# Kernel optimization log

Hardware: AMD Instinct MI355X
Metric: run time of the kernel (lower is better)

The kernel has to match this reference:

```python
import jax, jax.numpy as jnp
import numpy as np

B, S, D, H, L = 4, 2048, 256, 4, 2
DK = D // H
V, T = 32000, 1000


def setup_inputs() -> dict:
    key = jax.random.key(0)
    ks = jax.random.split(key, 20)
    sc = 0.02
    event_emb = jax.random.normal(ks[0], (V, D), jnp.float32) * sc
    event_emb = event_emb.at[0].set(0.0)  # padding_idx=0
    time_emb = jax.random.normal(ks[1], (T, D), jnp.float32) * sc
    inp = {
        "x": jax.random.randint(ks[2], (B, S), 0, V, jnp.int32),
        "time_deltas": jax.random.randint(ks[3], (B, S), 0, T, jnp.int32),
        "mask": jax.random.randint(ks[4], (B, S), 0, 2, jnp.int32),
        "event_emb": event_emb,
        "time_emb": time_emb,
        "Wq": jax.random.normal(ks[5], (L, D, D), jnp.float32) * sc,
        "bq": jnp.zeros((L, D), jnp.float32),
        "Wk": jax.random.normal(ks[6], (L, D, D), jnp.float32) * sc,
        "bk": jnp.zeros((L, D), jnp.float32),
        "Wv": jax.random.normal(ks[7], (L, D, D), jnp.float32) * sc,
        "bv": jnp.zeros((L, D), jnp.float32),
        "time_proj": jax.random.normal(ks[8], (L, T, H), jnp.float32) * sc,
        "Wo": jax.random.normal(ks[9], (L, D, D), jnp.float32) * sc,
        "bo": jnp.zeros((L, D), jnp.float32),
        "ln_g": jnp.ones((L, D), jnp.float32),
        "ln_b": jnp.zeros((L, D), jnp.float32),
        "Wc1": jax.random.normal(ks[10], (D, D // 2), jnp.float32) * sc,
        "bc1": jnp.zeros((D // 2,), jnp.float32),
        "Wc2": jax.random.normal(ks[11], (D // 2, 1), jnp.float32) * sc,
        "bc2": jnp.zeros((1,), jnp.float32),
    }
    return inp


def _layernorm(h, g, b, eps=1e-5):
    mu = jnp.mean(h, -1, keepdims=True)
    var = jnp.mean(jnp.square(h - mu), -1, keepdims=True)
    return (h - mu) * jax.lax.rsqrt(var + eps) * g + b


def _attn(h, t_bins, mask, Wq, bq, Wk, bk, Wv, bv, tp, Wo, bo):
    b, s, d = h.shape
    q = (h @ Wq + bq).reshape(b, s, H, DK)
    k = (h @ Wk + bk).reshape(b, s, H, DK)
    v = (h @ Wv + bv).reshape(b, s, H, DK)
    scores = jnp.einsum("bqhd,bkhd->bhqk", q, k) / np.sqrt(DK).astype(np.float32)
    time_bias = tp[t_bins]  # [b,s,H] -> bias per key position
    scores = scores + jnp.transpose(time_bias, (0, 2, 1))[:, :, None, :]
    scores = jnp.where(mask[:, None, None, :] == 0, -1e9, scores)
    attn = jax.nn.softmax(scores, axis=-1)
    ctx = jnp.einsum("bhqk,bkhd->bqhd", attn, v).reshape(b, s, d)
    return ctx @ Wo + bo


def reference(x, time_deltas, mask, event_emb, time_emb, Wq, bq, Wk, bk, Wv, bv,
              time_proj, Wo, bo, ln_g, ln_b, Wc1, bc1, Wc2, bc2):
    t_bins = jnp.clip(time_deltas, 0, T - 1)
    h = event_emb[x] + time_emb[t_bins]
    for l in range(L):
        h = _attn(h, t_bins, mask, Wq[l], bq[l], Wk[l], bk[l], Wv[l], bv[l],
                  time_proj[l], Wo[l], bo[l])
        h = _layernorm(h, ln_g[l], ln_b[l])
    last = h[:, -1, :]
    hid = jax.nn.relu(last @ Wc1 + bc1)
    return jax.nn.sigmoid(hid @ Wc2 + bc2)
```

## Files before the change

kernel.cpp:

```cpp
#include <hip/hip_runtime.h>
#include <math.h>

namespace {

constexpr int NB = 4, NS = 2048, ND = 256, NH = 4, NDK = 64, NL = 2, NT = 1000;
constexpr float L2E = 1.44269504089f;
constexpr float QSCALE = 0.125f * L2E;

typedef short bfx8 __attribute__((ext_vector_type(8)));
typedef float f32x4 __attribute__((ext_vector_type(4)));
typedef float f32x16 __attribute__((ext_vector_type(16)));

static __device__ __forceinline__ short f2bf(float f) {
  union { float f; unsigned u; } v; v.f = f;
  unsigned u = v.u;
  unsigned r = (u + 0x7fffu + ((u >> 16) & 1u)) >> 16;
  return (short)r;
}
static __device__ __forceinline__ float bf2f(short s) {
  union { float f; unsigned u; } v; v.u = ((unsigned)(unsigned short)s) << 16;
  return v.f;
}
static __device__ __forceinline__ float exp2_hw(float x) {
  float r;
  asm("v_exp_f32 %0, %1" : "=v"(r) : "v"(x));
  return r;
}
static __device__ __forceinline__ unsigned cvt_pk_bf16(float lo, float hi) {
  unsigned d;
  asm("v_cvt_pk_bf16_f32 %0, %1, %2" : "=v"(d) : "v"(lo), "v"(hi));
  return d;
}

__global__ __launch_bounds__(256) void k_packw(const float* __restrict__ Wq,
                                               const float* __restrict__ Wk,
                                               const float* __restrict__ Wv,
                                               const float* __restrict__ Wo,
                                               const float* __restrict__ bq,
                                               const float* __restrict__ bk,
                                               const float* __restrict__ bv,
                                               short* __restrict__ wqkvT,
                                               short* __restrict__ woT,
                                               float* __restrict__ bqkv) {
  __shared__ float t[64][65];
  int z = blockIdx.z, l = z >> 2, mat = z & 3;
  const float* src;
  short* dst;
  float scale = 1.f;
  if (mat == 0)      { src = Wq + (size_t)l * 65536; dst = wqkvT + (size_t)l * 768 * 256; scale = QSCALE; }
  else if (mat == 1) { src = Wk + (size_t)l * 65536; dst = wqkvT + (size_t)l * 768 * 256 + 256 * 256; }
  else if (mat == 2) { src = Wv + (size_t)l * 65536; dst = wqkvT + (size_t)l * 768 * 256 + 512 * 256; }
  else               { src = Wo + (size_t)l * 65536; dst = woT + (size_t)l * 65536; }
  int k0 = blockIdx.x * 64, n0 = blockIdx.y * 64;
  int c = threadIdx.x & 63, r4 = threadIdx.x >> 6;
  #pragma unroll
  for (int rr = 0; rr < 64; rr += 4) t[rr + r4][c] = src[(size_t)(k0 + rr + r4) * 256 + n0 + c];
  __syncthreads();
  #pragma unroll
  for (int rr = 0; rr < 64; rr += 4) {
    int n = rr + r4;
    dst[(size_t)(n0 + n) * 256 + k0 + c] = f2bf(t[c][n] * scale);
  }
  if (mat == 0 && blockIdx.x == 0 && blockIdx.y == 0) {
    for (int cc = threadIdx.x; cc < 768; cc += 256) {
      float v = cc < 256 ? bq[l * 256 + cc] * QSCALE
                         : (cc < 512 ? bk[l * 256 + cc - 256] : bv[l * 256 + cc - 512]);
      bqkv[l * 768 + cc] = v;
    }
  }
}

__global__ __launch_bounds__(256) void k_embed(const int* __restrict__ x,
                                               const int* __restrict__ td,
                                               const float* __restrict__ ee,
                                               const float* __restrict__ te,
                                               short* __restrict__ hb) {
  int lane = threadIdx.x & 63, r4 = threadIdx.x >> 6;
  int row = blockIdx.x * 4 + r4;
  int xi = x[row];
  int tb = td[row];
  tb = tb < 0 ? 0 : (tb >= NT ? NT - 1 : tb);
  float4 e = ((const float4*)&ee[(size_t)xi * ND])[lane];
  float4 tv = ((const float4*)&te[(size_t)tb * ND])[lane];
  short4 ob;
  ob.x = f2bf(e.x + tv.x); ob.y = f2bf(e.y + tv.y);
  ob.z = f2bf(e.z + tv.z); ob.w = f2bf(e.w + tv.w);
  ((short4*)&hb[(size_t)row * ND])[lane] = ob;
}

template <int OUT_BF16>
__global__ __launch_bounds__(256) void k_gemm(const short* __restrict__ A,
                                              const short* __restrict__ BT,
                                              const float* __restrict__ bias,
                                              void* __restrict__ C, int ldc,
                                              int mb_mul, int mb_add, int n_base) {
  constexpr int LP = 76;
  __shared__ short at[64][LP];
  __shared__ short bt[128][LP];
  int tid = threadIdx.x;
  int w = tid >> 6, lane = tid & 63, ln15 = lane & 15, g = lane >> 4;
  int m0 = (blockIdx.x * mb_mul + mb_add) * 64;
  int n0 = n_base + blockIdx.y * 128;
  int srow = tid >> 2, scol = (tid & 3) * 16;
  int brow = tid >> 1, bcol = (tid & 1) * 32;

  f32x4 acc[8];
  #pragma unroll
  for (int nt = 0; nt < 8; ++nt) acc[nt] = (f32x4){0.f, 0.f, 0.f, 0.f};

  bfx8 a0, a1, b0, b1, b2, b3;
  auto LOAD = [&](int kk0) {
    const short* as = &A[(size_t)(m0 + srow) * 256 + kk0 + scol];
    a0 = *(const bfx8*)as; a1 = *(const bfx8*)(as + 8);
    const short* bs = &BT[(size_t)(n0 + brow) * 256 + kk0 + bcol];
    b0 = *(const bfx8*)bs; b1 = *(const bfx8*)(bs + 8);
    b2 = *(const bfx8*)(bs + 16); b3 = *(const bfx8*)(bs + 24);
  };
  LOAD(0);
  for (int kk0 = 0; kk0 < 256; kk0 += 64) {
    __syncthreads();
    *(bfx8*)&at[srow][scol] = a0; *(bfx8*)&at[srow][scol + 8] = a1;
    *(bfx8*)&bt[brow][bcol] = b0; *(bfx8*)&bt[brow][bcol + 8] = b1;
    *(bfx8*)&bt[brow][bcol + 16] = b2; *(bfx8*)&bt[brow][bcol + 24] = b3;
    __syncthreads();
    if (kk0 + 64 < 256) LOAD(kk0 + 64);
    #pragma unroll
    for (int ks = 0; ks < 2; ++ks) {
      bfx8 af = *(const bfx8*)&at[w * 16 + ln15][ks * 32 + g * 8];
      #pragma unroll
      for (int nt = 0; nt < 8; ++nt) {
        bfx8 bf = *(const bfx8*)&bt[nt * 16 + ln15][ks * 32 + g * 8];
        acc[nt] = __builtin_amdgcn_mfma_f32_16x16x32_bf16(af, bf, acc[nt], 0, 0, 0);
      }
    }
  }

  #pragma unroll
  for (int nt = 0; nt < 8; ++nt) {
    int col = n0 + nt * 16 + ln15;
    float bb = bias[col];
    #pragma unroll
    for (int r = 0; r < 4; ++r) {
      int row = m0 + w * 16 + g * 4 + r;
      float val = acc[nt][r] + bb;
      if (OUT_BF16) ((short*)C)[(size_t)row * ldc + col] = f2bf(val);
      else          ((float*)C)[(size_t)row * ldc + col] = val;
    }
  }
}

__global__ __launch_bounds__(256) void k_pmerge(const short* __restrict__ partO,
                                                const float* __restrict__ partML,
                                                const short* __restrict__ BT,
                                                const float* __restrict__ bias,
                                                short* __restrict__ C) {
  constexpr int LP = 76;
  constexpr int NC = 2;
  __shared__ short at[64][LP];
  __shared__ short bt[128][LP];
  int tid = threadIdx.x;
  int w = tid >> 6, lane = tid & 63, ln15 = lane & 15, g = lane >> 4;
  int m0 = blockIdx.x * 64;
  int n0 = blockIdx.y * 128;
  int srow = tid >> 2, scol = (tid & 3) * 16;
  int brow = tid >> 1, bcol = (tid & 1) * 32;

  int grow = m0 + srow;
  int b = grow >> 11, s = grow & 2047;

  f32x4 acc[8];
  #pragma unroll
  for (int nt = 0; nt < 8; ++nt) acc[nt] = (f32x4){0.f, 0.f, 0.f, 0.f};

  bfx8 a0, a1, b0_, b1_, b2_, b3_;
  auto LOAD = [&](int kk0) {
    int hh2 = kk0 >> 6;
    size_t rbase = (size_t)(b * NH + hh2) * NS + s;
    float2 ml[NC];
    float M = -1e30f;
    #pragma unroll
    for (int c = 0; c < NC; ++c) {
      ml[c] = *(const float2*)&partML[(rbase + (size_t)c * 16 * NS) * 2];
      M = fmaxf(M, ml[c].x);
    }
    float wgt[NC], L = 0.f;
    #pragma unroll
    for (int c = 0; c < NC; ++c) { wgt[c] = exp2_hw(ml[c].x - M); L += ml[c].y * wgt[c]; }
    float inv = 1.f / L;
    float av[16];
    #pragma unroll
    for (int i = 0; i < 16; ++i) av[i] = 0.f;
    #pragma unroll
    for (int c = 0; c < NC; ++c) {
      float wc = wgt[c] * inv;
      size_t row = rbase + (size_t)c * 16 * NS;
      union { int4 v; short sh[8]; } ua, ub;
      ua.v = *(const int4*)&partO[row * 64 + scol];
      ub.v = *(const int4*)&partO[row * 64 + scol + 8];
      #pragma unroll
      for (int i = 0; i < 8; ++i) {
        av[i]     = fmaf(bf2f(ua.sh[i]), wc, av[i]);
        av[8 + i] = fmaf(bf2f(ub.sh[i]), wc, av[8 + i]);
      }
    }
    union { bfx8 v; short sh[8]; } pa, pb;
    #pragma unroll
    for (int i = 0; i < 8; ++i) { pa.sh[i] = f2bf(av[i]); pb.sh[i] = f2bf(av[8 + i]); }
    a0 = pa.v; a1 = pb.v;
    const short* bs = &BT[(size_t)(n0 + brow) * 256 + kk0 + bcol];
    b0_ = *(const bfx8*)bs; b1_ = *(const bfx8*)(bs + 8);
    b2_ = *(const bfx8*)(bs + 16); b3_ = *(const bfx8*)(bs + 24);
  };
  LOAD(0);
  for (int kk0 = 0; kk0 < 256; kk0 += 64) {
    __syncthreads();
    *(bfx8*)&at[srow][scol] = a0; *(bfx8*)&at[srow][scol + 8] = a1;
    *(bfx8*)&bt[brow][bcol] = b0_; *(bfx8*)&bt[brow][bcol + 8] = b1_;
    *(bfx8*)&bt[brow][bcol + 16] = b2_; *(bfx8*)&bt[brow][bcol + 24] = b3_;
    __syncthreads();
    if (kk0 + 64 < 256) LOAD(kk0 + 64);
    #pragma unroll
    for (int ks = 0; ks < 2; ++ks) {
      bfx8 af = *(const bfx8*)&at[w * 16 + ln15][ks * 32 + g * 8];
      #pragma unroll
      for (int nt = 0; nt < 8; ++nt) {
        bfx8 bf = *(const bfx8*)&bt[nt * 16 + ln15][ks * 32 + g * 8];
        acc[nt] = __builtin_amdgcn_mfma_f32_16x16x32_bf16(af, bf, acc[nt], 0, 0, 0);
      }
    }
  }

  #pragma unroll
  for (int nt = 0; nt < 8; ++nt) {
    int col = n0 + nt * 16 + ln15;
    float bb = bias[col];
    #pragma unroll
    for (int r = 0; r < 4; ++r) {
      int row = m0 + w * 16 + g * 4 + r;
      C[(size_t)row * 256 + col] = f2bf(acc[nt][r] + bb);
    }
  }
}

__global__ __launch_bounds__(256) void k_frag(const short* __restrict__ qkv,
                                              const int* __restrict__ td,
                                              const int* __restrict__ mask,
                                              const float* __restrict__ tp,
                                              short* __restrict__ vT,
                                              float* __restrict__ sbias_g) {
  __shared__ short vl[64][72];
  int tile = blockIdx.x, hh = blockIdx.y, b = blockIdx.z;
  int t = threadIdx.x;
  int k0 = tile * 64;
  {
    int key = t >> 2, dg = (t & 3) * 16;
    const short* vsrc = &qkv[(size_t)(b * NS + k0 + key) * 768 + 512 + hh * NDK + dg];
    bfx8 v0 = *(const bfx8*)vsrc, v1 = *(const bfx8*)(vsrc + 8);
    *(bfx8*)&vl[key][dg] = v0;
    *(bfx8*)&vl[key][dg + 8] = v1;
  }
  if (t < 64) {
    int kk = k0 + t;
    int tb = td[b * NS + kk];
    tb = tb < 0 ? 0 : (tb >= NT ? NT - 1 : tb);
    sbias_g[(size_t)(b * NH + hh) * NS + kk] = mask[b * NS + kk] ? tp[tb * NH + hh] * L2E : -1e9f;
  }
  __syncthreads();
  int dim = t >> 2, c0 = (t & 3) * 16;
  short outv[16];
  #pragma unroll
  for (int j = 0; j < 16; ++j) outv[j] = vl[c0 + j][dim];
  short* dst = &vT[(((size_t)(b * NH + hh) * 32 + tile) * 64 + dim) * 64 + c0];
  *(int4*)dst = *(const int4*)outv;
  *(int4*)(dst + 8) = *(const int4*)(outv + 8);
}

__global__ __launch_bounds__(256) void k_attn(const short* __restrict__ qkv,
                                              const short* __restrict__ vT,
                                              const float* __restrict__ sbias_g,
                                              short* __restrict__ partO,
                                              float* __restrict__ partML,
                                              int q_base, int qcount, int nchunk) {
  constexpr int LP = 76;
  __shared__ short kt[64][LP];
  __shared__ short vt[64][LP];
  __shared__ float sbias[64];

  int tid = threadIdx.x;
  int w = tid >> 6, lane = tid & 63, q31 = lane & 31, hl = lane >> 5;
  int b = blockIdx.z, hh = blockIdx.y;
  int bh = b * NH + hh;
  int qtile = blockIdx.x / nchunk;
  int chunk = blockIdx.x - qtile * nchunk;
  int niter = NS / (64 * nchunk);
  int tbase = chunk * niter;
  int q0 = q_base + qtile * 128;
  int qq = q0 + w * 32 + q31;

  bfx8 aq[4];
  #pragma unroll
  for (int ki = 0; ki < 4; ++ki)
    aq[ki] = *(const bfx8*)&qkv[(size_t)(b * NS + qq) * 768 + hh * NDK + ki * 16 + hl * 8];

  f32x16 o[2];
  #pragma unroll
  for (int dt = 0; dt < 2; ++dt)
    #pragma unroll
    for (int i = 0; i < 16; ++i) o[dt][i] = 0.f;
  float m = -1e30f, lsum = 0.f;

  int srow = tid >> 2, scg = (tid & 3) * 16;

  bfx8 kr0, kr1, vr0, vr1;
  float br = 0.f;
  auto loadset = [&](int it) {
    int tt = tbase + it;
    int k0 = tt * 64;
    const short* ksrc = &qkv[(size_t)(b * NS + k0 + srow) * 768 + 256 + hh * NDK + scg];
    kr0 = *(const bfx8*)ksrc; kr1 = *(const bfx8*)(ksrc + 8);
    const short* vsrc = &vT[(((size_t)bh * 32 + tt) * 64 + srow) * 64 + scg];
    vr0 = *(const bfx8*)vsrc; vr1 = *(const bfx8*)(vsrc + 8);
    if (tid < 64) br = sbias_g[(size_t)bh * NS + k0 + tid];
  };

  loadset(0);
  for (int it = 0; it < niter; ++it) {
    __syncthreads();
    *(bfx8*)&kt[srow][scg] = kr0;
    *(bfx8*)&kt[srow][scg + 8] = kr1;
    *(bfx8*)&vt[srow][scg] = vr0;
    *(bfx8*)&vt[srow][scg + 8] = vr1;
    if (tid < 64) sbias[tid] = br;
    __syncthreads();
    if (it + 1 < niter) loadset(it + 1);

    f32x16 c[2];
    #pragma unroll
    for (int kt2 = 0; kt2 < 2; ++kt2)
      #pragma unroll
      for (int i = 0; i < 16; ++i) c[kt2][i] = 0.f;
    __builtin_amdgcn_s_setprio(1);
    #pragma unroll
    for (int kt2 = 0; kt2 < 2; ++kt2) {
      #pragma unroll
      for (int ki = 0; ki < 4; ++ki) {
        bfx8 kf = *(const bfx8*)&kt[kt2 * 32 + q31][ki * 16 + hl * 8];
        c[kt2] = __builtin_amdgcn_mfma_f32_32x32x16_bf16(kf, aq[ki], c[kt2], 0, 0, 0);
      }
    }
    __builtin_amdgcn_s_setprio(0);

    #pragma unroll
    for (int kt2 = 0; kt2 < 2; ++kt2) {
      #pragma unroll
      for (int rg = 0; rg < 4; ++rg) {
        float4 bb = *(const float4*)&sbias[kt2 * 32 + rg * 8 + hl * 4];
        c[kt2][rg * 4 + 0] += bb.x; c[kt2][rg * 4 + 1] += bb.y;
        c[kt2][rg * 4 + 2] += bb.z; c[kt2][rg * 4 + 3] += bb.w;
      }
    }
    float rm = c[0][0];
    #pragma unroll
    for (int kt2 = 0; kt2 < 2; ++kt2)
      #pragma unroll
      for (int i = 0; i < 16; ++i) rm = fmaxf(rm, c[kt2][i]);
    rm = fmaxf(rm, __shfl_xor(rm, 32, 64));
    if (__any(rm > m + 10.f)) {
      float nm = fmaxf(m, rm);
      float scl = exp2_hw(m - nm);
      m = nm;
      lsum *= scl;
      #pragma unroll
      for (int dt = 0; dt < 2; ++dt)
        #pragma unroll
        for (int i = 0; i < 16; ++i) o[dt][i] *= scl;
    }
    float ts = 0.f;
    #pragma unroll
    for (int kt2 = 0; kt2 < 2; ++kt2)
      #pragma unroll
      for (int i = 0; i < 16; ++i) { c[kt2][i] = exp2_hw(c[kt2][i] - m); ts += c[kt2][i]; }
    lsum += ts;

    __builtin_amdgcn_s_setprio(1);
    #pragma unroll
    for (int kt2 = 0; kt2 < 2; ++kt2) {
      #pragma unroll
      for (int ks = 0; ks < 2; ++ks) {
        unsigned pa0 = cvt_pk_bf16(c[kt2][8 * ks + 0], c[kt2][8 * ks + 1]);
        unsigned pa1 = cvt_pk_bf16(c[kt2][8 * ks + 2], c[kt2][8 * ks + 3]);
        unsigned pb0 = cvt_pk_bf16(c[kt2][8 * ks + 4], c[kt2][8 * ks + 5]);
        unsigned pb1 = cvt_pk_bf16(c[kt2][8 * ks + 6], c[kt2][8 * ks + 7]);
        asm volatile("v_permlane32_swap_b32 %0, %1" : "+v"(pa0), "+v"(pb0));
        asm volatile("v_permlane32_swap_b32 %0, %1" : "+v"(pa1), "+v"(pb1));
        union { unsigned u[4]; bfx8 v; } pf;
        pf.u[0] = pa0; pf.u[1] = pa1; pf.u[2] = pb0; pf.u[3] = pb1;
        #pragma unroll
        for (int dt = 0; dt < 2; ++dt) {
          bfx8 vf = *(const bfx8*)&vt[dt * 32 + q31][kt2 * 32 + ks * 16 + hl * 8];
          o[dt] = __builtin_amdgcn_mfma_f32_32x32x16_bf16(vf, pf.v, o[dt], 0, 0, 0);
        }
      }
    }
    __builtin_amdgcn_s_setprio(0);
  }

  lsum += __shfl_xor(lsum, 32, 64);

  size_t rowi = (size_t)(chunk * 16 + bh) * qcount + qtile * 128 + w * 32 + q31;
  #pragma unroll
  for (int dt = 0; dt < 2; ++dt) {
    #pragma unroll
    for (int rg = 0; rg < 4; ++rg) {
      int2 pk;
      pk.x = (int)cvt_pk_bf16(o[dt][rg * 4 + 0], o[dt][rg * 4 + 1]);
      pk.y = (int)cvt_pk_bf16(o[dt][rg * 4 + 2], o[dt][rg * 4 + 3]);
      *(int2*)&partO[rowi * 64 + dt * 32 + rg * 8 + hl * 4] = pk;
    }
  }
  if (hl == 0) { partML[rowi * 2] = m; partML[rowi * 2 + 1] = lsum; }
}

__global__ __launch_bounds__(256) void k_amerge(const short* __restrict__ partO,
                                                const float* __restrict__ partML,
                                                short* __restrict__ ctx,
                                                int q_base, int qcount, int nchunk) {
  int b = blockIdx.z, hh = blockIdx.y;
  int qi = blockIdx.x * 64 + (threadIdx.x >> 2);
  int d0 = (threadIdx.x & 3) * 16;
  int bh = b * NH + hh;
  float M = -1e30f;
  for (int c = 0; c < nchunk; ++c)
    M = fmaxf(M, partML[((size_t)(c * 16 + bh) * qcount + qi) * 2]);
  float L = 0.f;
  float acc[16];
  #pragma unroll
  for (int i = 0; i < 16; ++i) acc[i] = 0.f;
  for (int c = 0; c < nchunk; ++c) {
    size_t row = (size_t)(c * 16 + bh) * qcount + qi;
    float mc = partML[row * 2];
    float lc = partML[row * 2 + 1];
    float s = exp2_hw(mc - M);
    L += lc * s;
    union { int4 v; short sh[8]; } u0, u1;
    u0.v = *(const int4*)&partO[row * 64 + d0];
    u1.v = *(const int4*)&partO[row * 64 + d0 + 8];
    #pragma unroll
    for (int i = 0; i < 8; ++i) {
      acc[i]     += bf2f(u0.sh[i]) * s;
      acc[8 + i] += bf2f(u1.sh[i]) * s;
    }
  }
  float inv = 1.f / L;
  short res[16];
  #pragma unroll
  for (int i = 0; i < 16; ++i) res[i] = f2bf(acc[i] * inv);
  short* dst = &ctx[(size_t)(b * NS + q_base + qi) * ND + hh * NDK + d0];
  *(int4*)dst = *(const int4*)res;
  *(int4*)(dst + 8) = *(const int4*)(res + 8);
}

__global__ __launch_bounds__(256) void k_ln(float* __restrict__ h,
                                            short* __restrict__ hb,
                                            const float* __restrict__ g_,
                                            const float* __restrict__ b_, int q_base) {
  int lane = threadIdx.x & 63, r4 = threadIdx.x >> 6;
  size_t row = (size_t)blockIdx.y * NS + q_base + blockIdx.x * 4 + r4;
  float4 v = ((const float4*)&h[row * ND])[lane];
  float s = v.x + v.y + v.z + v.w;
  #pragma unroll
  for (int off = 1; off < 64; off <<= 1) s += __shfl_xor(s, off, 64);
  float mu = s * (1.f / ND);
  float dx = v.x - mu, dy = v.y - mu, dz = v.z - mu, dw = v.w - mu;
  float q = dx * dx + dy * dy + dz * dz + dw * dw;
  #pragma unroll
  for (int off = 1; off < 64; off <<= 1) q += __shfl_xor(q, off, 64);
  float rr = rsqrtf(q * (1.f / ND) + 1e-5f);
  float4 gg = ((const float4*)g_)[lane];
  float4 bb = ((const float4*)b_)[lane];
  float4 o;
  o.x = dx * rr * gg.x + bb.x;
  o.y = dy * rr * gg.y + bb.y;
  o.z = dz * rr * gg.z + bb.z;
  o.w = dw * rr * gg.w + bb.w;
  ((float4*)&h[row * ND])[lane] = o;
  short4 ob; ob.x = f2bf(o.x); ob.y = f2bf(o.y); ob.z = f2bf(o.z); ob.w = f2bf(o.w);
  ((short4*)&hb[row * ND])[lane] = ob;
}

__global__ __launch_bounds__(256) void k_lnb(const short* __restrict__ in,
                                             short* __restrict__ hb,
                                             const float* __restrict__ g_,
                                             const float* __restrict__ b_) {
  int lane = threadIdx.x & 63, r4 = threadIdx.x >> 6;
  size_t row = (size_t)blockIdx.y * NS + blockIdx.x * 4 + r4;
  short4 sv = ((const short4*)&in[row * ND])[lane];
  float vx = bf2f(sv.x), vy = bf2f(sv.y), vz = bf2f(sv.z), vw = bf2f(sv.w);
  float s = vx + vy + vz + vw;
  #pragma unroll
  for (int off = 1; off < 64; off <<= 1) s += __shfl_xor(s, off, 64);
  float mu = s * (1.f / ND);
  float dx = vx - mu, dy = vy - mu, dz = vz - mu, dw = vw - mu;
  float q = dx * dx + dy * dy + dz * dz + dw * dw;
  #pragma unroll
  for (int off = 1; off < 64; off <<= 1) q += __shfl_xor(q, off, 64);
  float rr = rsqrtf(q * (1.f / ND) + 1e-5f);
  float4 gg = ((const float4*)g_)[lane];
  float4 bb = ((const float4*)b_)[lane];
  short4 ob;
  ob.x = f2bf(dx * rr * gg.x + bb.x);
  ob.y = f2bf(dy * rr * gg.y + bb.y);
  ob.z = f2bf(dz * rr * gg.z + bb.z);
  ob.w = f2bf(dw * rr * gg.w + bb.w);
  ((short4*)&hb[row * ND])[lane] = ob;
}

__global__ __launch_bounds__(128) void k_head(const float* __restrict__ h,
                                              const float* __restrict__ Wc1,
                                              const float* __restrict__ bc1,
                                              const float* __restrict__ Wc2,
                                              const float* __restrict__ bc2,
                                              float* __restrict__ out) {
  __shared__ float red[128];
  int j = threadIdx.x;
  int b = blockIdx.x;
  const float* last = &h[(size_t)(b * NS + NS - 1) * ND];
  float acc = bc1[j];
  for (int d = 0; d < ND; ++d) acc = fmaf(last[d], Wc1[d * 128 + j], acc);
  acc = fmaxf(acc, 0.f);
  red[j] = acc * Wc2[j];
  __syncthreads();
  for (int off = 64; off > 0; off >>= 1) {
    if (j < off) red[j] += red[j + off];
    __syncthreads();
  }
  if (j == 0) out[b] = 1.f / (1.f + __expf(-(red[0] + bc2[0])));
}

}

extern "C" void kernel_launch(void* const* d_in, const int* in_sizes, int n_in,
                              void* d_out, int out_size, void* d_ws, size_t ws_size,
                              hipStream_t stream) {
  const int* x = (const int*)d_in[0];
  const int* td = (const int*)d_in[1];
  const int* mask = (const int*)d_in[2];
  const float* ee = (const float*)d_in[3];
  const float* te = (const float*)d_in[4];
  const float* Wq = (const float*)d_in[5];
  const float* bq = (const float*)d_in[6];
  const float* Wk = (const float*)d_in[7];
  const float* bk = (const float*)d_in[8];
  const float* Wv = (const float*)d_in[9];
  const float* bv = (const float*)d_in[10];
  const float* tp = (const float*)d_in[11];
  const float* Wo = (const float*)d_in[12];
  const float* bo = (const float*)d_in[13];
  const float* lng = (const float*)d_in[14];
  const float* lnb = (const float*)d_in[15];
  const float* Wc1 = (const float*)d_in[16];
  const float* bc1 = (const float*)d_in[17];
  const float* Wc2 = (const float*)d_in[18];
  const float* bc2 = (const float*)d_in[19];
  float* out = (float*)d_out;

  char* ws = (char*)d_ws;
  const size_t M = (size_t)NB * NS;
  short* qkv     = (short*)(ws);
  float* h       = (float*)(ws + (12 << 20));
  short* hb      = (short*)(ws + (20 << 20));
  short* vT      = (short*)(ws + (24 << 20));
  float* sbias_g = (float*)(ws + (28 << 20));
  short* wqkvT   = (short*)(ws + (28 << 20) + (128 << 10));
  short* woT     = (short*)(ws + (28 << 20) + (896 << 10));
  float* bqkv    = (float*)(ws + (28 << 20) + (1152 << 10));
  short* partO   = (short*)(ws + (30 << 20));
  float* partML  = (float*)(ws + (47 << 20));
  short* hraw    = (short*)(ws + (48 << 20));
  short* ctx1    = vT;

  k_packw<<<dim3(4, 4, 8), 256, 0, stream>>>(Wq, Wk, Wv, Wo, bq, bk, bv, wqkvT, woT, bqkv);
  k_embed<<<NB * NS / 4, 256, 0, stream>>>(x, td, ee, te, hb);

  for (int l = 0; l < NL; ++l) {
    const short* wqkvTl = wqkvT + (size_t)l * 768 * 256;
    const short* woTl = woT + (size_t)l * 65536;
    const float* bqkvl = bqkv + (size_t)l * 768;
    const float* bol = bo + (size_t)l * ND;
    const float* tpl = tp + (size_t)l * NT * NH;
    const float* lngl = lng + (size_t)l * ND;
    const float* lnbl = lnb + (size_t)l * ND;
    const bool last = (l == NL - 1);

    if (!last) {
      k_gemm<1><<<dim3(M / 64, 6), 256, 0, stream>>>(hb, wqkvTl, bqkvl, qkv, 768, 1, 0, 0);
    } else {
      k_gemm<1><<<dim3(M / 64, 4), 256, 0, stream>>>(hb, wqkvTl, bqkvl, qkv, 768, 1, 0, 256);
      k_gemm<1><<<dim3(NB, 2), 256, 0, stream>>>(hb, wqkvTl, bqkvl, qkv, 768, 32, 31, 0);
    }

    k_frag<<<dim3(32, NH, NB), 256, 0, stream>>>(qkv, td, mask, tpl, vT, sbias_g);

    if (!last) {
      k_attn<<<dim3(16 * 2, NH, NB), 256, 0, stream>>>(qkv, vT, sbias_g,
                                                       partO, partML, 0, NS, 2);
      k_pmerge<<<dim3(M / 64, 2), 256, 0, stream>>>(partO, partML, woTl, bol, hraw);
      k_lnb<<<dim3(NS / 4, NB), 256, 0, stream>>>(hraw, hb, lngl, lnbl);
    } else {
      k_attn<<<dim3(16, NH, NB), 256, 0, stream>>>(qkv, vT, sbias_g,
                                                   partO, partML, NS - 128, 128, 16);
      k_amerge<<<dim3(2, NH, NB), 256, 0, stream>>>(partO, partML, ctx1, NS - 128, 128, 16);
      k_gemm<0><<<dim3(NB, 2), 256, 0, stream>>>(ctx1, woTl, bol, h, 256, 32, 31, 0);
      k_ln<<<dim3(1, NB), 256, 0, stream>>>(h, hb, lngl, lnbl, NS - 4);
    }
  }

  k_head<<<NB, 128, 0, stream>>>(h, Wc1, bc1, Wc2, bc2, out);
}
```

Measured before the change: 120.5 us.

## Fuse weight packing with embedding, merge+Wo GEMM, and LN with head

Merges weight packing and embedding gather into one launch, folds the last-layer split-KV merge into the Wo projection GEMM's A-operand load, and combines the final layernorm with the classifier head. Launch count drops from several small kernels to fewer. The aim is to remove launch overhead and intermediate ctx/h round trips on the tail, which is dominated by tiny grids. In exchange the merge work is recomputed per N-block in the GEMM, and the head now does LN with shared-memory reductions.

```diff
diff --git a/kernel.cpp b/kernel.cpp
--- a/kernel.cpp
+++ b/kernel.cpp
@@ -32,60 +32,62 @@
   return d;
 }
 
-__global__ __launch_bounds__(256) void k_packw(const float* __restrict__ Wq,
-                                               const float* __restrict__ Wk,
-                                               const float* __restrict__ Wv,
-                                               const float* __restrict__ Wo,
-                                               const float* __restrict__ bq,
-                                               const float* __restrict__ bk,
-                                               const float* __restrict__ bv,
-                                               short* __restrict__ wqkvT,
-                                               short* __restrict__ woT,
-                                               float* __restrict__ bqkv) {
-  __shared__ float t[64][65];
-  int z = blockIdx.z, l = z >> 2, mat = z & 3;
-  const float* src;
-  short* dst;
-  float scale = 1.f;
-  if (mat == 0)      { src = Wq + (size_t)l * 65536; dst = wqkvT + (size_t)l * 768 * 256; scale = QSCALE; }
-  else if (mat == 1) { src = Wk + (size_t)l * 65536; dst = wqkvT + (size_t)l * 768 * 256 + 256 * 256; }
-  else if (mat == 2) { src = Wv + (size_t)l * 65536; dst = wqkvT + (size_t)l * 768 * 256 + 512 * 256; }
-  else               { src = Wo + (size_t)l * 65536; dst = woT + (size_t)l * 65536; }
-  int k0 = blockIdx.x * 64, n0 = blockIdx.y * 64;
-  int c = threadIdx.x & 63, r4 = threadIdx.x >> 6;
-  #pragma unroll
-  for (int rr = 0; rr < 64; rr += 4) t[rr + r4][c] = src[(size_t)(k0 + rr + r4) * 256 + n0 + c];
-  __syncthreads();
-  #pragma unroll
-  for (int rr = 0; rr < 64; rr += 4) {
-    int n = rr + r4;
-    dst[(size_t)(n0 + n) * 256 + k0 + c] = f2bf(t[c][n] * scale);
-  }
-  if (mat == 0 && blockIdx.x == 0 && blockIdx.y == 0) {
-    for (int cc = threadIdx.x; cc < 768; cc += 256) {
-      float v = cc < 256 ? bq[l * 256 + cc] * QSCALE
-                         : (cc < 512 ? bk[l * 256 + cc - 256] : bv[l * 256 + cc - 512]);
-      bqkv[l * 768 + cc] = v;
-    }
-  }
-}
-
-__global__ __launch_bounds__(256) void k_embed(const int* __restrict__ x,
-                                               const int* __restrict__ td,
-                                               const float* __restrict__ ee,
-                                               const float* __restrict__ te,
-                                               short* __restrict__ hb) {
-  int lane = threadIdx.x & 63, r4 = threadIdx.x >> 6;
-  int row = blockIdx.x * 4 + r4;
-  int xi = x[row];
-  int tb = td[row];
-  tb = tb < 0 ? 0 : (tb >= NT ? NT - 1 : tb);
-  float4 e = ((const float4*)&ee[(size_t)xi * ND])[lane];
-  float4 tv = ((const float4*)&te[(size_t)tb * ND])[lane];
-  short4 ob;
-  ob.x = f2bf(e.x + tv.x); ob.y = f2bf(e.y + tv.y);
-  ob.z = f2bf(e.z + tv.z); ob.w = f2bf(e.w + tv.w);
-  ((short4*)&hb[(size_t)row * ND])[lane] = ob;
+__global__ __launch_bounds__(256) void k_packem(const int* __restrict__ x,
+                                                const int* __restrict__ td,
+                                                const float* __restrict__ ee,
+                                                const float* __restrict__ te,
+                                                short* __restrict__ hb,
+                                                const float* __restrict__ Wq,
+                                                const float* __restrict__ Wk,
+                                                const float* __restrict__ Wv,
+                                                const float* __restrict__ Wo,
+                                                const float* __restrict__ bq,
+                                                const float* __restrict__ bk,
+                                                const float* __restrict__ bv,
+                                                short* __restrict__ wqkvT,
+                                                short* __restrict__ woT,
+                                                float* __restrict__ bqkv) {
+  if (blockIdx.x < 128) {
+    __shared__ float t[64][65];
+    int bi = blockIdx.x;
+    int z = bi >> 4, l = z >> 2, mat = z & 3;
+    const float* src;
+    short* dst;
+    float scale = 1.f;
+    if (mat == 0)      { src = Wq + (size_t)l * 65536; dst = wqkvT + (size_t)l * 768 * 256; scale = QSCALE; }
+    else if (mat == 1) { src = Wk + (size_t)l * 65536; dst = wqkvT + (size_t)l * 768 * 256 + 256 * 256; }
+    else if (mat == 2) { src = Wv + (size_t)l * 65536; dst = wqkvT + (size_t)l * 768 * 256 + 512 * 256; }
+    else               { src = Wo + (size_t)l * 65536; dst = woT + (size_t)l * 65536; }
+    int k0 = (bi & 3) * 64, n0 = ((bi >> 2) & 3) * 64;
+    int c = threadIdx.x & 63, r4 = threadIdx.x >> 6;
+    #pragma unroll
+    for (int rr = 0; rr < 64; rr += 4) t[rr + r4][c] = src[(size_t)(k0 + rr + r4) * 256 + n0 + c];
+    __syncthreads();
+    #pragma unroll
+    for (int rr = 0; rr < 64; rr += 4) {
+      int n = rr + r4;
+      dst[(size_t)(n0 + n) * 256 + k0 + c] = f2bf(t[c][n] * scale);
+    }
+    if (mat == 0 && (bi & 15) == 0) {
+      for (int cc = threadIdx.x; cc < 768; cc += 256) {
+        float v = cc < 256 ? bq[l * 256 + cc] * QSCALE
+                           : (cc < 512 ? bk[l * 256 + cc - 256] : bv[l * 256 + cc - 512]);
+        bqkv[l * 768 + cc] = v;
+      }
+    }
+  } else {
+    int lane = threadIdx.x & 63, r4 = threadIdx.x >> 6;
+    int row = (blockIdx.x - 128) * 4 + r4;
+    int xi = x[row];
+    int tb = td[row];
+    tb = tb < 0 ? 0 : (tb >= NT ? NT - 1 : tb);
+    float4 e = ((const float4*)&ee[(size_t)xi * ND])[lane];
+    float4 tv = ((const float4*)&te[(size_t)tb * ND])[lane];
+    short4 ob;
+    ob.x = f2bf(e.x + tv.x); ob.y = f2bf(e.y + tv.y);
+    ob.z = f2bf(e.z + tv.z); ob.w = f2bf(e.w + tv.w);
+    ((short4*)&hb[(size_t)row * ND])[lane] = ob;
+  }
 }
 
 template <int OUT_BF16>
@@ -238,6 +240,101 @@
     for (int r = 0; r < 4; ++r) {
       int row = m0 + w * 16 + g * 4 + r;
       C[(size_t)row * 256 + col] = f2bf(acc[nt][r] + bb);
+    }
+  }
+}
+
+__global__ __launch_bounds__(256) void k_gmerge(const short* __restrict__ partO,
+                                                const float* __restrict__ partML,
+                                                const short* __restrict__ BT,
+                                                const float* __restrict__ bias,
+                                                float* __restrict__ C) {
+  constexpr int LP = 76;
+  constexpr int NC = 16;
+  __shared__ short at[64][LP];
+  __shared__ short bt[128][LP];
+  int tid = threadIdx.x;
+  int w = tid >> 6, lane = tid & 63, ln15 = lane & 15, g = lane >> 4;
+  int m0 = (blockIdx.x * 32 + 31) * 64;
+  int n0 = blockIdx.y * 128;
+  int srow = tid >> 2, scol = (tid & 3) * 16;
+  int brow = tid >> 1, bcol = (tid & 1) * 32;
+
+  int grow = m0 + srow;
+  int b = grow >> 11, s = grow & 2047;
+  int qloc = s - (NS - 128);
+
+  f32x4 acc[8];
+  #pragma unroll
+  for (int nt = 0; nt < 8; ++nt) acc[nt] = (f32x4){0.f, 0.f, 0.f, 0.f};
+
+  bfx8 a0, a1, b0_, b1_, b2_, b3_;
+  auto LOAD = [&](int kk0) {
+    int hh2 = kk0 >> 6;
+    size_t rbase = (size_t)(b * NH + hh2) * 128 + qloc;
+    float M = -1e30f;
+    float mls[NC], lls[NC];
+    #pragma unroll
+    for (int c = 0; c < NC; ++c) {
+      float2 ml = *(const float2*)&partML[(rbase + (size_t)c * 16 * 128) * 2];
+      mls[c] = ml.x; lls[c] = ml.y;
+      M = fmaxf(M, ml.x);
+    }
+    float L = 0.f, wgt[NC];
+    #pragma unroll
+    for (int c = 0; c < NC; ++c) { wgt[c] = exp2_hw(mls[c] - M); L += lls[c] * wgt[c]; }
+    float inv = 1.f / L;
+    float av[16];
+    #pragma unroll
+    for (int i = 0; i < 16; ++i) av[i] = 0.f;
+    #pragma unroll
+    for (int c = 0; c < NC; ++c) {
+      float wc = wgt[c] * inv;
+      size_t row = rbase + (size_t)c * 16 * 128;
+      union { int4 v; short sh[8]; } ua, ub;
+      ua.v = *(const int4*)&partO[row * 64 + scol];
+      ub.v = *(const int4*)&partO[row * 64 + scol + 8];
+      #pragma unroll
+      for (int i = 0; i < 8; ++i) {
+        av[i]     = fmaf(bf2f(ua.sh[i]), wc, av[i]);
+        av[8 + i] = fmaf(bf2f(ub.sh[i]), wc, av[8 + i]);
+      }
+    }
+    union { bfx8 v; short sh[8]; } pa, pb;
+    #pragma unroll
+    for (int i = 0; i < 8; ++i) { pa.sh[i] = f2bf(av[i]); pb.sh[i] = f2bf(av[8 + i]); }
+    a0 = pa.v; a1 = pb.v;
+    const short* bs = &BT[(size_t)(n0 + brow) * 256 + kk0 + bcol];
+    b0_ = *(const bfx8*)bs; b1_ = *(const bfx8*)(bs + 8);
+    b2_ = *(const bfx8*)(bs + 16); b3_ = *(const bfx8*)(bs + 24);
+  };
+  LOAD(0);
+  for (int kk0 = 0; kk0 < 256; kk0 += 64) {
+    __syncthreads();
+    *(bfx8*)&at[srow][scol] = a0; *(bfx8*)&at[srow][scol + 8] = a1;
+    *(bfx8*)&bt[brow][bcol] = b0_; *(bfx8*)&bt[brow][bcol + 8] = b1_;
+    *(bfx8*)&bt[brow][bcol + 16] = b2_; *(bfx8*)&bt[brow][bcol + 24] = b3_;
+    __syncthreads();
+    if (kk0 + 64 < 256) LOAD(kk0 + 64);
+    #pragma unroll
+    for (int ks = 0; ks < 2; ++ks) {
+      bfx8 af = *(const bfx8*)&at[w * 16 + ln15][ks * 32 + g * 8];
+      #pragma unroll
+      for (int nt = 0; nt < 8; ++nt) {
+        bfx8 bf = *(const bfx8*)&bt[nt * 16 + ln15][ks * 32 + g * 8];
+        acc[nt] = __builtin_amdgcn_mfma_f32_16x16x32_bf16(af, bf, acc[nt], 0, 0, 0);
+      }
+    }
+  }
+
+  #pragma unroll
+  for (int nt = 0; nt < 8; ++nt) {
+    int col = n0 + nt * 16 + ln15;
+    float bb = bias[col];
+    #pragma unroll
+    for (int r = 0; r < 4; ++r) {
+      int row = m0 + w * 16 + g * 4 + r;
+      C[(size_t)row * 256 + col] = acc[nt][r] + bb;
     }
   }
 }
@@ -421,73 +518,6 @@
   if (hl == 0) { partML[rowi * 2] = m; partML[rowi * 2 + 1] = lsum; }
 }
 
-__global__ __launch_bounds__(256) void k_amerge(const short* __restrict__ partO,
-                                                const float* __restrict__ partML,
-                                                short* __restrict__ ctx,
-                                                int q_base, int qcount, int nchunk) {
-  int b = blockIdx.z, hh = blockIdx.y;
-  int qi = blockIdx.x * 64 + (threadIdx.x >> 2);
-  int d0 = (threadIdx.x & 3) * 16;
-  int bh = b * NH + hh;
-  float M = -1e30f;
-  for (int c = 0; c < nchunk; ++c)
-    M = fmaxf(M, partML[((size_t)(c * 16 + bh) * qcount + qi) * 2]);
-  float L = 0.f;
-  float acc[16];
-  #pragma unroll
-  for (int i = 0; i < 16; ++i) acc[i] = 0.f;
-  for (int c = 0; c < nchunk; ++c) {
-    size_t row = (size_t)(c * 16 + bh) * qcount + qi;
-    float mc = partML[row * 2];
-    float lc = partML[row * 2 + 1];
-    float s = exp2_hw(mc - M);
-    L += lc * s;
-    union { int4 v; short sh[8]; } u0, u1;
-    u0.v = *(const int4*)&partO[row * 64 + d0];
-    u1.v = *(const int4*)&partO[row * 64 + d0 + 8];
-    #pragma unroll
-    for (int i = 0; i < 8; ++i) {
-      acc[i]     += bf2f(u0.sh[i]) * s;
-      acc[8 + i] += bf2f(u1.sh[i]) * s;
-    }
-  }
-  float inv = 1.f / L;
-  short res[16];
-  #pragma unroll
-  for (int i = 0; i < 16; ++i) res[i] = f2bf(acc[i] * inv);
-  short* dst = &ctx[(size_t)(b * NS + q_base + qi) * ND + hh * NDK + d0];
-  *(int4*)dst = *(const int4*)res;
-  *(int4*)(dst + 8) = *(const int4*)(res + 8);
-}
-
-__global__ __launch_bounds__(256) void k_ln(float* __restrict__ h,
-                                            short* __restrict__ hb,
-                                            const float* __restrict__ g_,
-                                            const float* __restrict__ b_, int q_base) {
-  int lane = threadIdx.x & 63, r4 = threadIdx.x >> 6;
-  size_t row = (size_t)blockIdx.y * NS + q_base + blockIdx.x * 4 + r4;
-  float4 v = ((const float4*)&h[row * ND])[lane];
-  float s = v.x + v.y + v.z + v.w;
-  #pragma unroll
-  for (int off = 1; off < 64; off <<= 1) s += __shfl_xor(s, off, 64);
-  float mu = s * (1.f / ND);
-  float dx = v.x - mu, dy = v.y - mu, dz = v.z - mu, dw = v.w - mu;
-  float q = dx * dx + dy * dy + dz * dz + dw * dw;
-  #pragma unroll
-  for (int off = 1; off < 64; off <<= 1) q += __shfl_xor(q, off, 64);
-  float rr = rsqrtf(q * (1.f / ND) + 1e-5f);
-  float4 gg = ((const float4*)g_)[lane];
-  float4 bb = ((const float4*)b_)[lane];
-  float4 o;
-  o.x = dx * rr * gg.x + bb.x;
-  o.y = dy * rr * gg.y + bb.y;
-  o.z = dz * rr * gg.z + bb.z;
-  o.w = dw * rr * gg.w + bb.w;
-  ((float4*)&h[row * ND])[lane] = o;
-  short4 ob; ob.x = f2bf(o.x); ob.y = f2bf(o.y); ob.z = f2bf(o.z); ob.w = f2bf(o.w);
-  ((short4*)&hb[row * ND])[lane] = ob;
-}
-
 __global__ __launch_bounds__(256) void k_lnb(const short* __restrict__ in,
                                              short* __restrict__ hb,
                                              const float* __restrict__ g_,
@@ -515,20 +545,44 @@
   ((short4*)&hb[row * ND])[lane] = ob;
 }
 
-__global__ __launch_bounds__(128) void k_head(const float* __restrict__ h,
-                                              const float* __restrict__ Wc1,
-                                              const float* __restrict__ bc1,
-                                              const float* __restrict__ Wc2,
-                                              const float* __restrict__ bc2,
-                                              float* __restrict__ out) {
-  __shared__ float red[128];
-  int j = threadIdx.x;
-  int b = blockIdx.x;
-  const float* last = &h[(size_t)(b * NS + NS - 1) * ND];
-  float acc = bc1[j];
-  for (int d = 0; d < ND; ++d) acc = fmaf(last[d], Wc1[d * 128 + j], acc);
-  acc = fmaxf(acc, 0.f);
-  red[j] = acc * Wc2[j];
+__global__ __launch_bounds__(256) void k_lnhead(const float* __restrict__ h,
+                                                const float* __restrict__ g_,
+                                                const float* __restrict__ b_,
+                                                const float* __restrict__ Wc1,
+                                                const float* __restrict__ bc1,
+                                                const float* __restrict__ Wc2,
+                                                const float* __restrict__ bc2,
+                                                float* __restrict__ out) {
+  __shared__ float rowv[256];
+  __shared__ float red[256];
+  int b = blockIdx.x, j = threadIdx.x;
+  float v = h[(size_t)(b * NS + NS - 1) * ND + j];
+  red[j] = v;
+  __syncthreads();
+  for (int off = 128; off > 0; off >>= 1) {
+    if (j < off) red[j] += red[j + off];
+    __syncthreads();
+  }
+  float mu = red[0] * (1.f / ND);
+  __syncthreads();
+  float d = v - mu;
+  red[j] = d * d;
+  __syncthreads();
+  for (int off = 128; off > 0; off >>= 1) {
+    if (j < off) red[j] += red[j + off];
+    __syncthreads();
+  }
+  float rr = rsqrtf(red[0] * (1.f / ND) + 1e-5f);
+  rowv[j] = d * rr * g_[j] + b_[j];
+  __syncthreads();
+  float hid = 0.f;
+  if (j < 128) {
+    hid = bc1[j];
+    for (int dd = 0; dd < ND; ++dd) hid = fmaf(rowv[dd], Wc1[dd * 128 + j], hid);
+    hid = fmaxf(hid, 0.f) * Wc2[j];
+  }
+  __syncthreads();
+  red[j] = j < 128 ? hid : 0.f;
   __syncthreads();
   for (int off = 64; off > 0; off >>= 1) {
     if (j < off) red[j] += red[j + off];
@@ -577,10 +631,10 @@
   short* partO   = (short*)(ws + (30 << 20));
   float* partML  = (float*)(ws + (47 << 20));
   short* hraw    = (short*)(ws + (48 << 20));
-  short* ctx1    = vT;
-
-  k_packw<<<dim3(4, 4, 8), 256, 0, stream>>>(Wq, Wk, Wv, Wo, bq, bk, bv, wqkvT, woT, bqkv);
-  k_embed<<<NB * NS / 4, 256, 0, stream>>>(x, td, ee, te, hb);
+
+  k_packem<<<128 + NB * NS / 4, 256, 0, stream>>>(x, td, ee, te, hb,
+                                                  Wq, Wk, Wv, Wo, bq, bk, bv,
+                                                  wqkvT, woT, bqkv);
 
   for (int l = 0; l < NL; ++l) {
     const short* wqkvTl = wqkvT + (size_t)l * 768 * 256;
@@ -609,11 +663,8 @@
     } else {
       k_attn<<<dim3(16, NH, NB), 256, 0, stream>>>(qkv, vT, sbias_g,
                                                    partO, partML, NS - 128, 128, 16);
-      k_amerge<<<dim3(2, NH, NB), 256, 0, stream>>>(partO, partML, ctx1, NS - 128, 128, 16);
-      k_gemm<0><<<dim3(NB, 2), 256, 0, stream>>>(ctx1, woTl, bol, h, 256, 32, 31, 0);
-      k_ln<<<dim3(1, NB), 256, 0, stream>>>(h, hb, lngl, lnbl, NS - 4);
-    }
-  }
-
-  k_head<<<NB, 128, 0, stream>>>(h, Wc1, bc1, Wc2, bc2, out);
-}
+      k_gmerge<<<dim3(NB, 2), 256, 0, stream>>>(partO, partML, woTl, bol, h);
+      k_lnhead<<<NB, 256, 0, stream>>>(h, lngl, lnbl, Wc1, bc1, Wc2, bc2, out);
+    }
+  }
+}
```

Result: faster. 117.3 us (median of 2 runs) (-2.7%).
